# Kernel tuning notes

Measured on AMD Instinct MI355X. Metric: run time of the kernel, lower is better.

The kernel has to match this reference:

```python
import jax, jax.numpy as jnp
import numpy as np

STRIDES = (8, 16, 32, 64, 128)
SCORE_THRESH = 0.05
IOU_THRESH = 0.6
MAX_DET = 1000


def _flat(p):
    # [B,C,H,W] -> [B,H*W,C]
    B, C = p.shape[0], p.shape[1]
    return jnp.transpose(p, (0, 2, 3, 1)).reshape(B, -1, C)


def _coords(h, w, stride):
    # FCOS coords_fmap2orig: center of each stride cell, (x, y) order -> [h*w, 2]
    sx = (jnp.arange(w, dtype=jnp.float32) * stride + stride // 2)
    sy = (jnp.arange(h, dtype=jnp.float32) * stride + stride // 2)
    yy, xx = jnp.meshgrid(sy, sx, indexing='ij')
    return jnp.stack([xx.ravel(), yy.ravel()], axis=-1)


def _nms_keep(boxes, valid, thr):
    # boxes: [M,4] sorted by descending score; valid: [M] bool. Greedy NMS keep mask.
    x1, y1, x2, y2 = boxes[:, 0], boxes[:, 1], boxes[:, 2], boxes[:, 3]
    area = (x2 - x1 + 1.0) * (y2 - y1 + 1.0)
    xx1 = jnp.maximum(x1[:, None], x1[None, :])
    yy1 = jnp.maximum(y1[:, None], y1[None, :])
    xx2 = jnp.minimum(x2[:, None], x2[None, :])
    yy2 = jnp.minimum(y2[:, None], y2[None, :])
    inter = jnp.clip(xx2 - xx1, 0.0) * jnp.clip(yy2 - yy1, 0.0)
    iou = inter / (area[:, None] + area[None, :] - inter)
    M = boxes.shape[0]
    idx = jnp.arange(M)

    def body(i, keep):
        sup = (idx > i) & (iou[i] > thr) & keep[i]
        return keep & (~sup)

    return jax.lax.fori_loop(0, M, body, valid)


def setup_inputs() -> dict:
    key = jax.random.key(0)
    B, C = 16, 80
    sizes = [(128, 128), (64, 64), (32, 32), (16, 16), (8, 8)]
    ks = jax.random.split(key, 15)
    inp = {}
    for i, (h, w) in enumerate(sizes):
        lvl = i + 3
        inp[f'cls_p{lvl}'] = jax.random.normal(ks[3 * i], (B, C, h, w), jnp.float32)
        inp[f'cnt_p{lvl}'] = jax.random.normal(ks[3 * i + 1], (B, 1, h, w), jnp.float32)
        inp[f'reg_p{lvl}'] = jax.random.uniform(ks[3 * i + 2], (B, 4, h, w), jnp.float32) * 100.0
    return inp


def _detect(cls_levels, cnt_levels, reg_levels):
    cls_logits = jnp.concatenate([_flat(p) for p in cls_levels], axis=1)  # [B,N,80]
    cnt_logits = jnp.concatenate([_flat(p) for p in cnt_levels], axis=1)  # [B,N,1]
    reg_preds = jnp.concatenate([_flat(p) for p in reg_levels], axis=1)   # [B,N,4]
    coords = jnp.concatenate(
        [_coords(p.shape[2], p.shape[3], s) for p, s in zip(cls_levels, STRIDES)], axis=0)  # [N,2]

    cls_preds = jax.nn.sigmoid(cls_logits)
    cnt_preds = jax.nn.sigmoid(cnt_logits)[..., 0]                        # [B,N]
    cls_max = jnp.max(cls_preds, axis=-1)                                 # [B,N]
    cls_classes = jnp.argmax(cls_preds, axis=-1) + 1                      # [B,N] 1-based labels
    scores = jnp.sqrt(cls_max * cnt_preds)                                # add_centerness

    boxes = jnp.concatenate(
        [coords[None] - reg_preds[..., :2], coords[None] + reg_preds[..., 2:]], axis=-1)  # [B,N,4]

    M = min(MAX_DET, scores.shape[1])
    topv, topi = jax.lax.top_k(scores, M)                                 # sorted desc
    classes_k = jnp.take_along_axis(cls_classes, topi, axis=1)            # [B,M]
    boxes_k = jnp.take_along_axis(boxes, topi[..., None], axis=1)         # [B,M,4]
    valid = topv >= SCORE_THRESH

    def per_image(b, s, c, v):
        # class-aware NMS via coordinate offset trick
        off = c.astype(b.dtype) * (jnp.max(b) + 1.0)
        keep = _nms_keep(b + off[:, None], v, IOU_THRESH)
        kf = keep.astype(s.dtype)
        return s * kf, c * keep.astype(c.dtype), b * kf[:, None]

    return jax.vmap(per_image)(boxes_k, topv, classes_k, valid)


def reference(cls_p3, cnt_p3, reg_p3, cls_p4, cnt_p4, reg_p4, cls_p5, cnt_p5, reg_p5,
              cls_p6, cnt_p6, reg_p6, cls_p7, cnt_p7, reg_p7):
    cls_levels = [cls_p3, cls_p4, cls_p5, cls_p6, cls_p7]
    cnt_levels = [cnt_p3, cnt_p4, cnt_p5, cnt_p6, cnt_p7]
    reg_levels = [reg_p3, reg_p4, reg_p5, reg_p6, reg_p7]
    return _detect(cls_levels, cnt_levels, reg_levels)
```

## Files before the change

### kernel.cpp

```cpp
#include <hip/hip_runtime.h>
#include <hip/hip_bf16.h>
#include <math.h>

#define NB 16
#define NC 80
#define NA 21824
#define NM 1000
#define NHBINS 16384
#define CANDCAP 4096

#define OFF_KEYS     0ul
#define OFF_CLSV     2793472ul
#define OFF_HIST     4190208ul
#define OFF_CANDCNT  5238784ul
#define OFF_MAXB     5238848ul
#define OFF_CANDS    5238912ul
#define OFF_TOPSCORE 5763200ul
#define OFF_TOPCLS   5827200ul
#define OFF_TOPBOX   5891200ul
#define OFF_MASK     6147200ul

__device__ __forceinline__ float sigm(float x) { return 1.0f / (1.0f + expf(-x)); }

__global__ __launch_bounds__(256, 4) void k_score(
    const float* __restrict__ cls3, const float* __restrict__ cnt3,
    const float* __restrict__ cls4, const float* __restrict__ cnt4,
    const float* __restrict__ cls5, const float* __restrict__ cnt5,
    const float* __restrict__ cls6, const float* __restrict__ cnt6,
    const float* __restrict__ cls7, const float* __restrict__ cnt7,
    unsigned long long* __restrict__ keys,
    float* __restrict__ clsv, unsigned int* __restrict__ hist)
{
    __shared__ unsigned int histpk[NHBINS / 2];
    __shared__ float lm[4 * 64 * 4];
    __shared__ int   lam[4 * 64 * 4];
    __shared__ float cm[256];
    __shared__ int   cam[256];
    const int b = blockIdx.y;
    const int tid = threadIdx.x;
    const int a = tid & 63, s = tid >> 6;
    const int g4 = blockIdx.x * 64 + a;

    for (int i = tid; i < NHBINS / 2; i += 256) histpk[i] = 0u;

    if (g4 < (NA >> 2)) {
        const int n = g4 << 2;
        const float* clsP; int off, logW;
        if      (n < 16384) { clsP = cls3; off = 0;     logW = 7; }
        else if (n < 20480) { clsP = cls4; off = 16384; logW = 6; }
        else if (n < 21504) { clsP = cls5; off = 20480; logW = 5; }
        else if (n < 21760) { clsP = cls6; off = 21504; logW = 4; }
        else                { clsP = cls7; off = 21760; logW = 3; }
        const int HW4 = 1 << (2 * logW - 2);
        const int l4 = (n - off) >> 2;
        const float4* cp = (const float4*)clsP + (size_t)b * NC * HW4 + l4;
        const int c0 = s * 20;
        float4 v[20];
#pragma unroll
        for (int u = 0; u < 20; u++) v[u] = cp[(size_t)(c0 + u) * HW4];
        float m[4] = { v[0].x, v[0].y, v[0].z, v[0].w };
        int am[4] = { c0, c0, c0, c0 };
#pragma unroll
        for (int u = 1; u < 20; u++) {
            const int c = c0 + u;
            if (v[u].x > m[0]) { m[0] = v[u].x; am[0] = c; }
            if (v[u].y > m[1]) { m[1] = v[u].y; am[1] = c; }
            if (v[u].z > m[2]) { m[2] = v[u].z; am[2] = c; }
            if (v[u].w > m[3]) { m[3] = v[u].w; am[3] = c; }
        }
#pragma unroll
        for (int k = 0; k < 4; k++) { lm[tid * 4 + k] = m[k]; lam[tid * 4 + k] = am[k]; }
    }
    __syncthreads();
    if (tid < 64 && (blockIdx.x * 64 + tid) < (NA >> 2)) {
        float M[4]; int AM[4];
#pragma unroll
        for (int k = 0; k < 4; k++) { M[k] = lm[tid * 4 + k]; AM[k] = lam[tid * 4 + k]; }
        for (int s2 = 1; s2 < 4; s2++) {
#pragma unroll
            for (int k = 0; k < 4; k++) {
                float vv = lm[(s2 * 64 + tid) * 4 + k];
                if (vv > M[k]) { M[k] = vv; AM[k] = lam[(s2 * 64 + tid) * 4 + k]; }
            }
        }
#pragma unroll
        for (int k = 0; k < 4; k++) { cm[tid * 4 + k] = M[k]; cam[tid * 4 + k] = AM[k]; }
    }
    __syncthreads();
    const int n2 = blockIdx.x * 256 + tid;
    if (n2 < NA) {
        const float* cntP; int off, logW;
        if      (n2 < 16384) { cntP = cnt3; off = 0;     logW = 7; }
        else if (n2 < 20480) { cntP = cnt4; off = 16384; logW = 6; }
        else if (n2 < 21504) { cntP = cnt5; off = 20480; logW = 5; }
        else if (n2 < 21760) { cntP = cnt6; off = 21504; logW = 4; }
        else                 { cntP = cnt7; off = 21760; logW = 3; }
        const int HW = 1 << (2 * logW);
        const int local = n2 - off;
        float cn = cntP[(size_t)b * HW + local];
        float M = cm[tid]; int AM = cam[tid];
        float sc = sqrtf(sigm(M) * sigm(cn));
        unsigned long long key = ((unsigned long long)__float_as_uint(sc) << 32)
                               | (unsigned int)(~(unsigned int)n2);
        keys[(size_t)b * NA + n2] = key;
        unsigned int bin = (unsigned int)(key >> 50);
        atomicAdd(&histpk[bin >> 1], (bin & 1u) ? 0x10000u : 1u);
        clsv[(size_t)b * NA + n2] = (float)(AM + 1);
    }
    __syncthreads();
    unsigned int* gh = hist + b * NHBINS;
    for (int i = tid; i < NHBINS / 2; i += 256) {
        unsigned int pk = histpk[i];
        if (pk) {
            unsigned int lo = pk & 0xFFFFu, hi = pk >> 16;
            if (lo) atomicAdd(&gh[2 * i], lo);
            if (hi) atomicAdd(&gh[2 * i + 1], hi);
        }
    }
}

__global__ __launch_bounds__(256) void k_compact(
    const unsigned long long* __restrict__ keys, const unsigned int* __restrict__ hist,
    unsigned int* __restrict__ candcnt, unsigned long long* __restrict__ cands)
{
    __shared__ int part1[256];
    __shared__ int part2[8];
    __shared__ int sBoundary;
    __shared__ unsigned int lcount;
    __shared__ unsigned int lbase;
    const int b = blockIdx.y;
    const int tid = threadIdx.x;
    const unsigned int* h = hist + b * NHBINS;
    int sum = 0;
    for (int i = 0; i < 64; i++) sum += (int)h[tid * 64 + i];
    part1[tid] = sum;
    if (tid == 0) lcount = 0u;
    __syncthreads();
    if (tid < 8) { int s2 = 0; for (int t = 0; t < 32; t++) s2 += part1[tid * 32 + t]; part2[tid] = s2; }
    __syncthreads();
    if (tid == 0) {
        int acc = 0, sc;
        for (sc = 7; sc > 0; sc--) { if (acc + part2[sc] >= NM) break; acc += part2[sc]; }
        int t;
        for (t = sc * 32 + 31; t > sc * 32; t--) { if (acc + part1[t] >= NM) break; acc += part1[t]; }
        int bin;
        for (bin = t * 64 + 63; bin > t * 64; bin--) { if (acc + (int)h[bin] >= NM) break; acc += (int)h[bin]; }
        sBoundary = bin;
    }
    __syncthreads();
    const unsigned int boundary = (unsigned int)sBoundary;
    unsigned long long hk[4]; unsigned int hslot[4]; int nh = 0;
    for (int nn = blockIdx.x * 256 + tid; nn < NA; nn += 22 * 256) {
        unsigned long long key = keys[(size_t)b * NA + nn];
        if ((unsigned int)(key >> 50) >= boundary) {
            hslot[nh] = atomicAdd(&lcount, 1u);
            hk[nh] = key;
            nh++;
        }
    }
    __syncthreads();
    if (tid == 0) lbase = atomicAdd(&candcnt[b], lcount);
    __syncthreads();
    const unsigned int base = lbase;
    for (int t = 0; t < nh; t++) {
        unsigned int pos = base + hslot[t];
        if (pos < CANDCAP) cands[(size_t)b * CANDCAP + pos] = hk[t];
    }
}

__global__ __launch_bounds__(256) void k_rank(
    const unsigned long long* __restrict__ cands, const unsigned int* __restrict__ candcnt,
    const float* __restrict__ clsv,
    const float* __restrict__ reg3, const float* __restrict__ reg4, const float* __restrict__ reg5,
    const float* __restrict__ reg6, const float* __restrict__ reg7,
    float* __restrict__ topscore, float* __restrict__ topcls,
    float4* __restrict__ topbox, unsigned int* __restrict__ maxbEnc)
{
    __shared__ unsigned long long sbuf[CANDCAP];
    __shared__ unsigned int redmax[256];
    const int b = blockIdx.y;
    int cnt = (int)candcnt[b]; if (cnt > CANDCAP) cnt = CANDCAP;
    const int base = blockIdx.x * 256;
    if (base >= cnt) return;
    const int tid = threadIdx.x;
    for (int i = tid; i < cnt; i += 256) sbuf[i] = cands[(size_t)b * CANDCAP + i];
    __syncthreads();
    const int idx = base + tid;
    unsigned int enc = 0;
    if (idx < cnt) {
        const unsigned long long key = sbuf[idx];
        const unsigned int ai = ~(unsigned int)key;
        const float* regP; int off, W, logW, st;
        if      (ai < 16384) { regP = reg3; off = 0;     W = 128; logW = 7; st = 8;   }
        else if (ai < 20480) { regP = reg4; off = 16384; W = 64;  logW = 6; st = 16;  }
        else if (ai < 21504) { regP = reg5; off = 20480; W = 32;  logW = 5; st = 32;  }
        else if (ai < 21760) { regP = reg6; off = 21504; W = 16;  logW = 4; st = 64;  }
        else                 { regP = reg7; off = 21760; W = 8;   logW = 3; st = 128; }
        const int local = (int)ai - off;
        const int HW = 1 << (2 * logW);
        const float* rp = regP + (size_t)b * 4 * HW + local;
        float r0 = rp[0], r1 = rp[HW], r2 = rp[2 * HW], r3 = rp[3 * HW];
        float cv = clsv[(size_t)b * NA + ai];
        int rank = 0;
        int j = 0;
        for (; j + 4 <= cnt; j += 4) {
            rank += (sbuf[j] > key) + (sbuf[j+1] > key) + (sbuf[j+2] > key) + (sbuf[j+3] > key);
        }
        for (; j < cnt; j++) rank += (sbuf[j] > key);
        if (rank < NM) {
            const float hs = (float)(st >> 1);
            float cx = (float)((local & (W - 1)) * st) + hs;
            float cy = (float)((local >> logW) * st) + hs;
            float4 bx = make_float4(cx - r0, cy - r1, cx + r2, cy + r3);
            topscore[b * NM + rank] = __uint_as_float((unsigned int)(key >> 32));
            topcls[b * NM + rank] = cv;
            topbox[b * NM + rank] = bx;
            float mx = fmaxf(fmaxf(bx.x, bx.y), fmaxf(bx.z, bx.w));
            unsigned int ub = __float_as_uint(mx);
            enc = (ub & 0x80000000u) ? ~ub : (ub | 0x80000000u);
        }
    }
    redmax[tid] = enc;
    __syncthreads();
    for (int sgap = 128; sgap > 0; sgap >>= 1) {
        if (tid < sgap) { unsigned int o = redmax[tid + sgap]; if (o > redmax[tid]) redmax[tid] = o; }
        __syncthreads();
    }
    if (tid == 0 && redmax[0]) atomicMax(&maxbEnc[b], redmax[0]);
}

__global__ __launch_bounds__(256) void k_iou(
    const float4* __restrict__ topbox, const float* __restrict__ topcls,
    const unsigned int* __restrict__ maxbEnc, unsigned long long* __restrict__ maskArr)
{
    __shared__ float4 sB[NM];
    __shared__ float sA[NM];
    const int b = blockIdx.y;
    const int tid = threadIdx.x;
    unsigned int enc = maxbEnc[b];
    unsigned int ub = (enc & 0x80000000u) ? (enc & 0x7FFFFFFFu) : ~enc;
    const float mp1 = __fadd_rn(__uint_as_float(ub), 1.0f);
    for (int r = tid; r < NM; r += 256) {
        float4 f = topbox[b * NM + r];
        float off = __fmul_rn(topcls[b * NM + r], mp1);
        f.x = __fadd_rn(f.x, off); f.y = __fadd_rn(f.y, off);
        f.z = __fadd_rn(f.z, off); f.w = __fadd_rn(f.w, off);
        sB[r] = f;
        sA[r] = __fmul_rn(__fadd_rn(__fsub_rn(f.z, f.x), 1.0f),
                          __fadd_rn(__fsub_rn(f.w, f.y), 1.0f));
    }
    __syncthreads();
    int task = blockIdx.x * 256 + tid;
    if (task >= NM * 16) return;
    int w = task / NM, i = task - w * NM;
    float4 bi = sB[i]; float ai = sA[i];
    unsigned long long bits = 0ULL;
    int j0 = w << 6;
    int jstart = (j0 > i + 1) ? j0 : i + 1;
    int jend = (j0 + 64 < NM) ? j0 + 64 : NM;
    for (int j = jstart; j < jend; j++) {
        float4 bj = sB[j];
        float xx1 = fmaxf(bi.x, bj.x);
        float yy1 = fmaxf(bi.y, bj.y);
        float xx2 = fminf(bi.z, bj.z);
        float yy2 = fminf(bi.w, bj.w);
        float iw = fmaxf(__fsub_rn(xx2, xx1), 0.0f);
        float ih = fmaxf(__fsub_rn(yy2, yy1), 0.0f);
        float inter = __fmul_rn(iw, ih);
        float denom = __fsub_rn(__fadd_rn(ai, sA[j]), inter);
        float iou = inter / denom;
        if (iou > 0.6f) bits |= (1ULL << (j - j0));
    }
    maskArr[((size_t)b * 16 + w) * NM + i] = bits;
}

__global__ __launch_bounds__(256) void k_nms_sweep(
    const unsigned long long* __restrict__ maskArr,
    const float* __restrict__ topscore, const float* __restrict__ topcls,
    const float4* __restrict__ topbox, float* __restrict__ out)
{
    __shared__ unsigned long long smask[16 * NM];
    __shared__ unsigned long long lremv[16];
    const int b = blockIdx.x;
    const int tid = threadIdx.x;
    const int j = tid & 63, q = tid >> 6;
    const unsigned long long* gmask = maskArr + (size_t)b * (16 * NM);

    {
        const ulonglong2* src = (const ulonglong2*)gmask;
        ulonglong2* dst = (ulonglong2*)smask;
        for (int idx = tid; idx < 8 * NM; idx += 256) dst[idx] = src[idx];
    }
    if (tid < 16) lremv[tid] = 0ULL;
    __syncthreads();
    for (int r = tid; r < NM; r += 256) {
        float s = topscore[b * NM + r];
        if (!(s >= 0.05f)) atomicOr(&lremv[r >> 6], 1ULL << (r & 63));
    }

    for (int w = 0; w < 16; w++) {
        __syncthreads();
        const int row = w * 64 + j;
        unsigned long long D = (row < NM) ? smask[w * NM + row] : 0ULL;
        unsigned int dlo = (unsigned int)D, dhi = (unsigned int)(D >> 32);
        unsigned long long sv = lremv[w];
        unsigned int slo = __builtin_amdgcn_readfirstlane((unsigned int)sv);
        unsigned int shi = __builtin_amdgcn_readfirstlane((unsigned int)(sv >> 32));
        unsigned long long s = ((unsigned long long)shi << 32) | slo;
#pragma unroll
        for (int bb = 0; bb < 64; bb++) {
            unsigned int rlo = __builtin_amdgcn_readlane(dlo, bb);
            unsigned int rhi = __builtin_amdgcn_readlane(dhi, bb);
            unsigned long long rowv = ((unsigned long long)rhi << 32) | rlo;
            unsigned long long t = s | rowv;
            s = ((s >> bb) & 1ULL) ? s : t;
        }
        if (tid == 0) lremv[w] = s;
        const unsigned long long kw = ~s;
        if ((kw >> j) & 1ULL) {
            for (int k = w + 1 + q; k < 16; k += 4) {
                unsigned long long v = (row < NM) ? smask[k * NM + row] : 0ULL;
                if (v) atomicOr(&lremv[k], v);
            }
        }
    }
    __syncthreads();

    for (int r = tid; r < NM; r += 256) {
        bool keep = !((lremv[r >> 6] >> (r & 63)) & 1ULL);
        float kf = keep ? 1.0f : 0.0f;
        out[b * NM + r] = topscore[b * NM + r] * kf;
        out[NB * NM + b * NM + r] = topcls[b * NM + r] * kf;
        float4 bx = topbox[b * NM + r];
        ((float4*)(out + 2 * NB * NM))[b * NM + r] = make_float4(bx.x * kf, bx.y * kf, bx.z * kf, bx.w * kf);
    }
}

extern "C" void kernel_launch(void* const* d_in, const int* in_sizes, int n_in,
                              void* d_out, int out_size, void* d_ws, size_t ws_size,
                              hipStream_t stream) {
    const float* cls3 = (const float*)d_in[0];
    const float* cnt3 = (const float*)d_in[1];
    const float* reg3 = (const float*)d_in[2];
    const float* cls4 = (const float*)d_in[3];
    const float* cnt4 = (const float*)d_in[4];
    const float* reg4 = (const float*)d_in[5];
    const float* cls5 = (const float*)d_in[6];
    const float* cnt5 = (const float*)d_in[7];
    const float* reg5 = (const float*)d_in[8];
    const float* cls6 = (const float*)d_in[9];
    const float* cnt6 = (const float*)d_in[10];
    const float* reg6 = (const float*)d_in[11];
    const float* cls7 = (const float*)d_in[12];
    const float* cnt7 = (const float*)d_in[13];
    const float* reg7 = (const float*)d_in[14];

    char* ws = (char*)d_ws;
    unsigned long long* keys   = (unsigned long long*)(ws + OFF_KEYS);
    float*              clsv   = (float*)(ws + OFF_CLSV);
    unsigned int*       hist   = (unsigned int*)(ws + OFF_HIST);
    unsigned int*       candcnt= (unsigned int*)(ws + OFF_CANDCNT);
    unsigned int*       maxbE  = (unsigned int*)(ws + OFF_MAXB);
    unsigned long long* cands  = (unsigned long long*)(ws + OFF_CANDS);
    float*              topsc  = (float*)(ws + OFF_TOPSCORE);
    float*              topcl  = (float*)(ws + OFF_TOPCLS);
    float4*             topbx  = (float4*)(ws + OFF_TOPBOX);
    unsigned long long* maskA  = (unsigned long long*)(ws + OFF_MASK);

    hipMemsetAsync(ws + OFF_HIST, 0, (size_t)(NB * NHBINS * 4 + 128), stream);

    dim3 g1(86, NB);
    k_score<<<g1, 256, 0, stream>>>(cls3, cnt3, cls4, cnt4, cls5, cnt5,
                                    cls6, cnt6, cls7, cnt7,
                                    keys, clsv, hist);
    dim3 g2(22, NB);
    k_compact<<<g2, 256, 0, stream>>>(keys, hist, candcnt, cands);
    dim3 g3(CANDCAP / 256, NB);
    k_rank<<<g3, 256, 0, stream>>>(cands, candcnt, clsv, reg3, reg4, reg5, reg6, reg7,
                                   topsc, topcl, topbx, maxbE);
    dim3 g4(63, NB);
    k_iou<<<g4, 256, 0, stream>>>(topbx, topcl, maxbE, maskA);
    k_nms_sweep<<<NB, 256, 0, stream>>>(maskA, topsc, topcl, topbx, (float*)d_out);
}
```

Measured before the change: 270.9 us.

## Fuse IoU and NMS sweep into one per-image kernel, shrink histogram

Merges the IoU bitmask kernel and the NMS sweep into a single 1024-thread block per image that computes masks directly into shared memory, removing a launch and the global mask round-trip. Shrinks the score histogram from 16384 to 2048 bins to reduce clearing and scanning, and streams class loads through a 4-deep register buffer to allow higher occupancy in the scoring kernel. Risks: IoU work now runs on only one block per image, and coarser bins may push more candidates past the boundary, possibly overflowing the candidate buffer.

```diff
diff --git a/kernel.cpp b/kernel.cpp
--- a/kernel.cpp
+++ b/kernel.cpp
@@ -6,23 +6,22 @@
 #define NC 80
 #define NA 21824
 #define NM 1000
-#define NHBINS 16384
+#define NHBINS 2048
 #define CANDCAP 4096
 
 #define OFF_KEYS     0ul
 #define OFF_CLSV     2793472ul
 #define OFF_HIST     4190208ul
-#define OFF_CANDCNT  5238784ul
-#define OFF_MAXB     5238848ul
-#define OFF_CANDS    5238912ul
-#define OFF_TOPSCORE 5763200ul
-#define OFF_TOPCLS   5827200ul
-#define OFF_TOPBOX   5891200ul
-#define OFF_MASK     6147200ul
+#define OFF_CANDCNT  4321280ul
+#define OFF_MAXB     4321344ul
+#define OFF_CANDS    4321408ul
+#define OFF_TOPSCORE 4845696ul
+#define OFF_TOPCLS   4909696ul
+#define OFF_TOPBOX   4973696ul
 
 __device__ __forceinline__ float sigm(float x) { return 1.0f / (1.0f + expf(-x)); }
 
-__global__ __launch_bounds__(256, 4) void k_score(
+__global__ __launch_bounds__(256, 6) void k_score(
     const float* __restrict__ cls3, const float* __restrict__ cnt3,
     const float* __restrict__ cls4, const float* __restrict__ cnt4,
     const float* __restrict__ cls5, const float* __restrict__ cnt5,
@@ -55,18 +54,20 @@
         const int l4 = (n - off) >> 2;
         const float4* cp = (const float4*)clsP + (size_t)b * NC * HW4 + l4;
         const int c0 = s * 20;
-        float4 v[20];
-#pragma unroll
-        for (int u = 0; u < 20; u++) v[u] = cp[(size_t)(c0 + u) * HW4];
-        float m[4] = { v[0].x, v[0].y, v[0].z, v[0].w };
+        float4 buf[4];
+#pragma unroll
+        for (int u = 0; u < 4; u++) buf[u] = cp[(size_t)(c0 + u) * HW4];
+        float m[4] = { -3.402823466e+38f, -3.402823466e+38f, -3.402823466e+38f, -3.402823466e+38f };
         int am[4] = { c0, c0, c0, c0 };
 #pragma unroll
-        for (int u = 1; u < 20; u++) {
+        for (int u = 0; u < 20; u++) {
+            float4 vv = buf[u & 3];
+            if (u + 4 < 20) buf[u & 3] = cp[(size_t)(c0 + u + 4) * HW4];
             const int c = c0 + u;
-            if (v[u].x > m[0]) { m[0] = v[u].x; am[0] = c; }
-            if (v[u].y > m[1]) { m[1] = v[u].y; am[1] = c; }
-            if (v[u].z > m[2]) { m[2] = v[u].z; am[2] = c; }
-            if (v[u].w > m[3]) { m[3] = v[u].w; am[3] = c; }
+            if (vv.x > m[0]) { m[0] = vv.x; am[0] = c; }
+            if (vv.y > m[1]) { m[1] = vv.y; am[1] = c; }
+            if (vv.z > m[2]) { m[2] = vv.z; am[2] = c; }
+            if (vv.w > m[3]) { m[3] = vv.w; am[3] = c; }
         }
 #pragma unroll
         for (int k = 0; k < 4; k++) { lm[tid * 4 + k] = m[k]; lam[tid * 4 + k] = am[k]; }
@@ -103,7 +104,7 @@
         unsigned long long key = ((unsigned long long)__float_as_uint(sc) << 32)
                                | (unsigned int)(~(unsigned int)n2);
         keys[(size_t)b * NA + n2] = key;
-        unsigned int bin = (unsigned int)(key >> 50);
+        unsigned int bin = (unsigned int)(key >> 51);
         atomicAdd(&histpk[bin >> 1], (bin & 1u) ? 0x10000u : 1u);
         clsv[(size_t)b * NA + n2] = (float)(AM + 1);
     }
@@ -132,7 +133,7 @@
     const int tid = threadIdx.x;
     const unsigned int* h = hist + b * NHBINS;
     int sum = 0;
-    for (int i = 0; i < 64; i++) sum += (int)h[tid * 64 + i];
+    for (int i = 0; i < 8; i++) sum += (int)h[tid * 8 + i];
     part1[tid] = sum;
     if (tid == 0) lcount = 0u;
     __syncthreads();
@@ -144,7 +145,7 @@
         int t;
         for (t = sc * 32 + 31; t > sc * 32; t--) { if (acc + part1[t] >= NM) break; acc += part1[t]; }
         int bin;
-        for (bin = t * 64 + 63; bin > t * 64; bin--) { if (acc + (int)h[bin] >= NM) break; acc += (int)h[bin]; }
+        for (bin = t * 8 + 7; bin > t * 8; bin--) { if (acc + (int)h[bin] >= NM) break; acc += (int)h[bin]; }
         sBoundary = bin;
     }
     __syncthreads();
@@ -152,7 +153,7 @@
     unsigned long long hk[4]; unsigned int hslot[4]; int nh = 0;
     for (int nn = blockIdx.x * 256 + tid; nn < NA; nn += 22 * 256) {
         unsigned long long key = keys[(size_t)b * NA + nn];
-        if ((unsigned int)(key >> 50) >= boundary) {
+        if ((unsigned int)(key >> 51) >= boundary) {
             hslot[nh] = atomicAdd(&lcount, 1u);
             hk[nh] = key;
             nh++;
@@ -229,74 +230,62 @@
     if (tid == 0 && redmax[0]) atomicMax(&maxbEnc[b], redmax[0]);
 }
 
-__global__ __launch_bounds__(256) void k_iou(
+__global__ __launch_bounds__(1024, 1) void k_tail(
     const float4* __restrict__ topbox, const float* __restrict__ topcls,
-    const unsigned int* __restrict__ maxbEnc, unsigned long long* __restrict__ maskArr)
-{
-    __shared__ float4 sB[NM];
-    __shared__ float sA[NM];
-    const int b = blockIdx.y;
-    const int tid = threadIdx.x;
-    unsigned int enc = maxbEnc[b];
-    unsigned int ub = (enc & 0x80000000u) ? (enc & 0x7FFFFFFFu) : ~enc;
-    const float mp1 = __fadd_rn(__uint_as_float(ub), 1.0f);
-    for (int r = tid; r < NM; r += 256) {
-        float4 f = topbox[b * NM + r];
-        float off = __fmul_rn(topcls[b * NM + r], mp1);
-        f.x = __fadd_rn(f.x, off); f.y = __fadd_rn(f.y, off);
-        f.z = __fadd_rn(f.z, off); f.w = __fadd_rn(f.w, off);
-        sB[r] = f;
-        sA[r] = __fmul_rn(__fadd_rn(__fsub_rn(f.z, f.x), 1.0f),
-                          __fadd_rn(__fsub_rn(f.w, f.y), 1.0f));
-    }
-    __syncthreads();
-    int task = blockIdx.x * 256 + tid;
-    if (task >= NM * 16) return;
-    int w = task / NM, i = task - w * NM;
-    float4 bi = sB[i]; float ai = sA[i];
-    unsigned long long bits = 0ULL;
-    int j0 = w << 6;
-    int jstart = (j0 > i + 1) ? j0 : i + 1;
-    int jend = (j0 + 64 < NM) ? j0 + 64 : NM;
-    for (int j = jstart; j < jend; j++) {
-        float4 bj = sB[j];
-        float xx1 = fmaxf(bi.x, bj.x);
-        float yy1 = fmaxf(bi.y, bj.y);
-        float xx2 = fminf(bi.z, bj.z);
-        float yy2 = fminf(bi.w, bj.w);
-        float iw = fmaxf(__fsub_rn(xx2, xx1), 0.0f);
-        float ih = fmaxf(__fsub_rn(yy2, yy1), 0.0f);
-        float inter = __fmul_rn(iw, ih);
-        float denom = __fsub_rn(__fadd_rn(ai, sA[j]), inter);
-        float iou = inter / denom;
-        if (iou > 0.6f) bits |= (1ULL << (j - j0));
-    }
-    maskArr[((size_t)b * 16 + w) * NM + i] = bits;
-}
-
-__global__ __launch_bounds__(256) void k_nms_sweep(
-    const unsigned long long* __restrict__ maskArr,
-    const float* __restrict__ topscore, const float* __restrict__ topcls,
-    const float4* __restrict__ topbox, float* __restrict__ out)
+    const float* __restrict__ topscore, const unsigned int* __restrict__ maxbEnc,
+    float* __restrict__ out)
 {
     __shared__ unsigned long long smask[16 * NM];
+    __shared__ float4 sB[NM];
+    __shared__ float  sA[NM];
     __shared__ unsigned long long lremv[16];
     const int b = blockIdx.x;
     const int tid = threadIdx.x;
     const int j = tid & 63, q = tid >> 6;
-    const unsigned long long* gmask = maskArr + (size_t)b * (16 * NM);
-
-    {
-        const ulonglong2* src = (const ulonglong2*)gmask;
-        ulonglong2* dst = (ulonglong2*)smask;
-        for (int idx = tid; idx < 8 * NM; idx += 256) dst[idx] = src[idx];
+
+    unsigned int enc = maxbEnc[b];
+    unsigned int ub = (enc & 0x80000000u) ? (enc & 0x7FFFFFFFu) : ~enc;
+    const float mp1 = __fadd_rn(__uint_as_float(ub), 1.0f);
+
+    float myscore = 0.f, mycls = 0.f;
+    float4 mybox = make_float4(0.f, 0.f, 0.f, 0.f);
+    if (tid < NM) {
+        myscore = topscore[b * NM + tid];
+        mycls = topcls[b * NM + tid];
+        mybox = topbox[b * NM + tid];
+        float off = __fmul_rn(mycls, mp1);
+        float4 f = make_float4(__fadd_rn(mybox.x, off), __fadd_rn(mybox.y, off),
+                               __fadd_rn(mybox.z, off), __fadd_rn(mybox.w, off));
+        sB[tid] = f;
+        sA[tid] = __fmul_rn(__fadd_rn(__fsub_rn(f.z, f.x), 1.0f),
+                            __fadd_rn(__fsub_rn(f.w, f.y), 1.0f));
     }
     if (tid < 16) lremv[tid] = 0ULL;
     __syncthreads();
-    for (int r = tid; r < NM; r += 256) {
-        float s = topscore[b * NM + r];
-        if (!(s >= 0.05f)) atomicOr(&lremv[r >> 6], 1ULL << (r & 63));
-    }
+
+    for (int t = tid; t < 16 * NM; t += 1024) {
+        int w = t / NM, i = t - w * NM;
+        float4 bi = sB[i]; float ai = sA[i];
+        unsigned long long bits = 0ULL;
+        int j0 = w << 6;
+        int jstart = (j0 > i + 1) ? j0 : i + 1;
+        int jend = (j0 + 64 < NM) ? j0 + 64 : NM;
+        for (int jj = jstart; jj < jend; jj++) {
+            float4 bj = sB[jj];
+            float xx1 = fmaxf(bi.x, bj.x);
+            float yy1 = fmaxf(bi.y, bj.y);
+            float xx2 = fminf(bi.z, bj.z);
+            float yy2 = fminf(bi.w, bj.w);
+            float iw = fmaxf(__fsub_rn(xx2, xx1), 0.0f);
+            float ih = fmaxf(__fsub_rn(yy2, yy1), 0.0f);
+            float inter = __fmul_rn(iw, ih);
+            float denom = __fsub_rn(__fadd_rn(ai, sA[jj]), inter);
+            float iou = inter / denom;
+            if (iou > 0.6f) bits |= (1ULL << (jj - j0));
+        }
+        smask[w * NM + i] = bits;
+    }
+    if (tid < NM && !(myscore >= 0.05f)) atomicOr(&lremv[tid >> 6], 1ULL << (tid & 63));
 
     for (int w = 0; w < 16; w++) {
         __syncthreads();
@@ -318,7 +307,7 @@
         if (tid == 0) lremv[w] = s;
         const unsigned long long kw = ~s;
         if ((kw >> j) & 1ULL) {
-            for (int k = w + 1 + q; k < 16; k += 4) {
+            for (int k = w + 1 + q; k < 16; k += 16) {
                 unsigned long long v = (row < NM) ? smask[k * NM + row] : 0ULL;
                 if (v) atomicOr(&lremv[k], v);
             }
@@ -326,13 +315,13 @@
     }
     __syncthreads();
 
-    for (int r = tid; r < NM; r += 256) {
-        bool keep = !((lremv[r >> 6] >> (r & 63)) & 1ULL);
+    if (tid < NM) {
+        bool keep = !((lremv[tid >> 6] >> (tid & 63)) & 1ULL);
         float kf = keep ? 1.0f : 0.0f;
-        out[b * NM + r] = topscore[b * NM + r] * kf;
-        out[NB * NM + b * NM + r] = topcls[b * NM + r] * kf;
-        float4 bx = topbox[b * NM + r];
-        ((float4*)(out + 2 * NB * NM))[b * NM + r] = make_float4(bx.x * kf, bx.y * kf, bx.z * kf, bx.w * kf);
+        out[b * NM + tid] = myscore * kf;
+        out[NB * NM + b * NM + tid] = mycls * kf;
+        ((float4*)(out + 2 * NB * NM))[b * NM + tid] =
+            make_float4(mybox.x * kf, mybox.y * kf, mybox.z * kf, mybox.w * kf);
     }
 }
 
@@ -365,7 +354,6 @@
     float*              topsc  = (float*)(ws + OFF_TOPSCORE);
     float*              topcl  = (float*)(ws + OFF_TOPCLS);
     float4*             topbx  = (float4*)(ws + OFF_TOPBOX);
-    unsigned long long* maskA  = (unsigned long long*)(ws + OFF_MASK);
 
     hipMemsetAsync(ws + OFF_HIST, 0, (size_t)(NB * NHBINS * 4 + 128), stream);
 
@@ -378,7 +366,5 @@
     dim3 g3(CANDCAP / 256, NB);
     k_rank<<<g3, 256, 0, stream>>>(cands, candcnt, clsv, reg3, reg4, reg5, reg6, reg7,
                                    topsc, topcl, topbx, maxbE);
-    dim3 g4(63, NB);
-    k_iou<<<g4, 256, 0, stream>>>(topbx, topcl, maxbE, maskA);
-    k_nms_sweep<<<NB, 256, 0, stream>>>(maskA, topsc, topcl, topbx, (float*)d_out);
-}
+    k_tail<<<NB, 1024, 0, stream>>>(topbx, topcl, topsc, maxbE, (float*)d_out);
+}
```

Result: slower. 412.9 us (+52.4%).
